# Optimization experiments

Hardware: AMD Instinct MI355X
Metric: run time of the kernel (lower is better)

Reference implementation:

```python
import jax, jax.numpy as jnp
import numpy as np

B, S, D = 2, 2048, 1024
H = 16
DH = D // H
DFF = 4096
EPS = 1e-5


def _layer_norm(x, gamma, beta):
    mu = jnp.mean(x, axis=-1, keepdims=True)
    var = jnp.mean(jnp.square(x - mu), axis=-1, keepdims=True)
    return (x - mu) * jax.lax.rsqrt(var + EPS) * gamma + beta


def setup_inputs() -> dict:
    key = jax.random.key(0)
    ks = jax.random.split(key, 8)
    sc_d = 1.0 / np.sqrt(D)
    sc_f = 1.0 / np.sqrt(DFF)
    x = jax.random.normal(ks[0], (B, S, D), dtype=jnp.float32)
    mask = jnp.ones((B, 1, 1, S), dtype=jnp.int32)
    # attention projections (stored as (in, out); y = x @ W + b)
    Wq = jax.random.normal(ks[1], (D, D), dtype=jnp.float32) * sc_d
    Wk = jax.random.normal(ks[2], (D, D), dtype=jnp.float32) * sc_d
    Wv = jax.random.normal(ks[3], (D, D), dtype=jnp.float32) * sc_d
    Wo = jax.random.normal(ks[4], (D, D), dtype=jnp.float32) * sc_d
    bq = jnp.zeros((D,), jnp.float32)
    bk = jnp.zeros((D,), jnp.float32)
    bv = jnp.zeros((D,), jnp.float32)
    bo = jnp.zeros((D,), jnp.float32)
    # feed-forward
    W0 = jax.random.normal(ks[5], (D, DFF), dtype=jnp.float32) * sc_d
    b0 = jnp.zeros((DFF,), jnp.float32)
    W1 = jax.random.normal(ks[6], (DFF, D), dtype=jnp.float32) * sc_f
    b1 = jnp.zeros((D,), jnp.float32)
    # layer norms
    g0 = jnp.ones((D,), jnp.float32)
    be0 = jnp.zeros((D,), jnp.float32)
    g1 = jnp.ones((D,), jnp.float32)
    be1 = jnp.zeros((D,), jnp.float32)
    return dict(x=x, mask=mask, Wq=Wq, bq=bq, Wk=Wk, bk=bk, Wv=Wv, bv=bv,
                Wo=Wo, bo=bo, W0=W0, b0=b0, W1=W1, b1=b1,
                g0=g0, be0=be0, g1=g1, be1=be1)


def reference(x, mask, Wq, bq, Wk, bk, Wv, bv, Wo, bo, W0, b0, W1, b1, g0, be0, g1, be1):
    b, s, d = x.shape
    # --- multi-head self-attention ---
    q = (x @ Wq + bq).reshape(b, s, H, DH).transpose(0, 2, 1, 3)  # (b,h,s,dh)
    k = (x @ Wk + bk).reshape(b, s, H, DH).transpose(0, 2, 1, 3)
    v = (x @ Wv + bv).reshape(b, s, H, DH).transpose(0, 2, 1, 3)
    scores = jnp.einsum('bhqd,bhkd->bhqk', q, k) / np.sqrt(DH)  # (b,h,s,s)
    scores = jnp.where(mask == 0, jnp.float32(-1e9), scores)
    probs = jax.nn.softmax(scores, axis=-1)
    ctx = jnp.einsum('bhqk,bhkd->bhqd', probs, v)
    ctx = ctx.transpose(0, 2, 1, 3).reshape(b, s, d)
    attn_out = ctx @ Wo + bo
    # dropout is identity in eval mode
    h0 = _layer_norm(x + attn_out, g0, be0)
    # --- feed-forward ---
    ff = jax.nn.relu(h0 @ W0 + b0) @ W1 + b1
    return _layer_norm(h0 + ff, g1, be1)
```

## Files before the change

kernel.cpp:

```cpp
#include <hip/hip_runtime.h>
#include <stdint.h>

#define B_ 2
#define S_ 2048
#define D_ 1024
#define H_ 16
#define DH_ 64
#define DFF_ 4096
#define NROW_ (B_*S_)
#define KVB_ 64

typedef __attribute__((ext_vector_type(8))) short bf16x8;
typedef __attribute__((ext_vector_type(4))) float f32x4;
typedef __attribute__((ext_vector_type(16))) float f32x16;
typedef __attribute__((ext_vector_type(4))) unsigned int u32x4;

__device__ __forceinline__ float bf2f(unsigned short u) {
  union { unsigned int i; float f; } v; v.i = ((unsigned int)u) << 16; return v.f;
}
__device__ __forceinline__ unsigned short f2bf(float f) {
  union { float f; unsigned int i; } v; v.f = f;
  unsigned int r = v.i + 0x7fffu + ((v.i >> 16) & 1u);
  return (unsigned short)(r >> 16);
}

__device__ __forceinline__ void gload16(const void* g, void* l) {
  __builtin_amdgcn_global_load_lds(
      (const __attribute__((address_space(1))) unsigned int*)(uintptr_t)g,
      (__attribute__((address_space(3))) unsigned int*)(unsigned int)(uintptr_t)l,
      16, 0, 0);
}

__device__ __forceinline__ void xcd_swz(int& bx, int& by) {
  const int gx = gridDim.x, nwg = gx * gridDim.y;
  const int flat = blockIdx.y * gx + blockIdx.x;
  const int chunk = nwg >> 3;
  const int nf = (flat & 7) * chunk + (flat >> 3);
  bx = nf % gx; by = nf / gx;
}

__global__ __launch_bounds__(256)
void k_cvt(const float* __restrict__ in, unsigned short* __restrict__ out, int n) {
  int i = (blockIdx.x * 256 + threadIdx.x) * 4;
  if (i < n) {
    float4 f = *(const float4*)(in + i);
    ushort4 o; o.x = f2bf(f.x); o.y = f2bf(f.y); o.z = f2bf(f.z); o.w = f2bf(f.w);
    *(ushort4*)(out + i) = o;
  }
}

__global__ __launch_bounds__(256)
void k_cat3(const float* __restrict__ a, const float* __restrict__ b,
            const float* __restrict__ c, float* __restrict__ o) {
  int i = blockIdx.x * 256 + threadIdx.x;
  if (i < 3 * D_)
    o[i] = i < D_ ? a[i] : (i < 2 * D_ ? b[i - D_] : c[i - 2 * D_]);
}

__global__ __launch_bounds__(256)
void k_cvt_t(const float* __restrict__ in, unsigned short* __restrict__ out,
             int K, int N) {
  __shared__ float tile[32][33];
  const int k0 = blockIdx.y * 32, n0 = blockIdx.x * 32;
  const int tx = threadIdx.x & 31, ty = threadIdx.x >> 5;
  #pragma unroll
  for (int i = 0; i < 32; i += 8)
    tile[ty + i][tx] = in[(size_t)(k0 + ty + i) * N + n0 + tx];
  __syncthreads();
  #pragma unroll
  for (int i = 0; i < 32; i += 8)
    out[(size_t)(n0 + ty + i) * K + k0 + tx] = f2bf(tile[tx][ty + i]);
}

__global__ __launch_bounds__(256)
void k_tr_v(const unsigned short* __restrict__ v, unsigned short* __restrict__ vt) {
  __shared__ unsigned short tile[32][33];
  const int b = blockIdx.z;
  const int s0 = blockIdx.y * 32, c0 = blockIdx.x * 32;
  const int tx = threadIdx.x & 31, ty = threadIdx.x >> 5;
  #pragma unroll
  for (int i = 0; i < 32; i += 8)
    tile[ty + i][tx] = v[((size_t)(b * S_ + s0 + ty + i)) * D_ + c0 + tx];
  __syncthreads();
  #pragma unroll
  for (int i = 0; i < 32; i += 8)
    vt[((size_t)(b * D_ + c0 + ty + i)) * S_ + s0 + tx] = tile[tx][ty + i];
}

template<int EPI>
__global__ __launch_bounds__(256, 2)
void k_gemm(const unsigned short* __restrict__ A,
            const unsigned short* __restrict__ Bt,
            const float* __restrict__ bias,
            void* __restrict__ out, int M, int N, int K) {
  __shared__ unsigned short Al[128 * 64];
  __shared__ unsigned short Bl[128 * 64];
  const int tid = threadIdx.x;
  const int wave = tid >> 6, l = tid & 63;
  int bx, by; xcd_swz(bx, by);
  const int m0 = by * 128, n0 = bx * 128;
  const int wm = (wave >> 1) * 64, wn = (wave & 1) * 64;
  const int g = l >> 4, c = l & 15;
  f32x4 acc[4][4] = {};
  const int srow = wave * 8 + (l >> 3);
  const int scol = (l & 7) * 8;

  for (int kt = 0; kt < K; kt += 64) {
    #pragma unroll
    for (int p = 0; p < 4; ++p) {
      const int r = p * 32 + srow;
      gload16(A + (size_t)(m0 + r) * K + kt + scol, Al + r * 64 + scol);
      gload16(Bt + (size_t)(n0 + r) * K + kt + scol, Bl + r * 64 + scol);
    }
    __syncthreads();
    #pragma unroll
    for (int ks = 0; ks < 2; ++ks) {
      bf16x8 af[4], bf[4];
      #pragma unroll
      for (int i = 0; i < 4; ++i) {
        af[i] = *(const bf16x8*)(Al + (wm + i * 16 + c) * 64 + ks * 32 + g * 8);
        bf[i] = *(const bf16x8*)(Bl + (wn + i * 16 + c) * 64 + ks * 32 + g * 8);
      }
      #pragma unroll
      for (int i = 0; i < 4; ++i)
        #pragma unroll
        for (int j = 0; j < 4; ++j)
          acc[i][j] = __builtin_amdgcn_mfma_f32_16x16x32_bf16(af[i], bf[j], acc[i][j], 0, 0, 0);
    }
    __syncthreads();
  }

  #pragma unroll
  for (int j = 0; j < 4; ++j) {
    const int col = n0 + wn + j * 16 + c;
    const float bv = bias[col];
    #pragma unroll
    for (int i = 0; i < 4; ++i) {
      #pragma unroll
      for (int r = 0; r < 4; ++r) {
        const int row = m0 + wm + i * 16 + g * 4 + r;
        float v = acc[i][j][r] + bv;
        if (EPI == 1) v = v > 0.f ? v : 0.f;
        if (EPI == 2) {
          ((float*)out)[(size_t)row * N + col] = v;
        } else if (EPI == 3) {
          ((unsigned short*)out)[(size_t)(col >> 10) * ((size_t)NROW_ * D_) +
                                 (size_t)row * D_ + (col & (D_ - 1))] = f2bf(v);
        } else {
          ((unsigned short*)out)[(size_t)row * N + col] = f2bf(v);
        }
      }
    }
  }
}

__global__ __launch_bounds__(256, 2)
void k_gemm_sk(const unsigned short* __restrict__ A,
               const unsigned short* __restrict__ Bt,
               const float* __restrict__ bias,
               unsigned short* __restrict__ out, int M, int N, int K, int KCH) {
  __shared__ unsigned short Al[128 * 64];
  __shared__ unsigned short Bl[128 * 64];
  const int tid = threadIdx.x;
  const int wave = tid >> 6, l = tid & 63;
  int bx, by; xcd_swz(bx, by);
  const int m0 = by * 128, n0 = bx * 128;
  const int kbeg = blockIdx.z * KCH;
  const int wm = (wave >> 1) * 64, wn = (wave & 1) * 64;
  const int g = l >> 4, c = l & 15;
  f32x4 acc[4][4] = {};
  const int srow = wave * 8 + (l >> 3);
  const int scol = (l & 7) * 8;

  for (int kt = kbeg; kt < kbeg + KCH; kt += 64) {
    #pragma unroll
    for (int p = 0; p < 4; ++p) {
      const int r = p * 32 + srow;
      gload16(A + (size_t)(m0 + r) * K + kt + scol, Al + r * 64 + scol);
      gload16(Bt + (size_t)(n0 + r) * K + kt + scol, Bl + r * 64 + scol);
    }
    __syncthreads();
    #pragma unroll
    for (int ks = 0; ks < 2; ++ks) {
      bf16x8 af[4], bf[4];
      #pragma unroll
      for (int i = 0; i < 4; ++i) {
        af[i] = *(const bf16x8*)(Al + (wm + i * 16 + c) * 64 + ks * 32 + g * 8);
        bf[i] = *(const bf16x8*)(Bl + (wn + i * 16 + c) * 64 + ks * 32 + g * 8);
      }
      #pragma unroll
      for (int i = 0; i < 4; ++i)
        #pragma unroll
        for (int j = 0; j < 4; ++j)
          acc[i][j] = __builtin_amdgcn_mfma_f32_16x16x32_bf16(af[i], bf[j], acc[i][j], 0, 0, 0);
    }
    __syncthreads();
  }

  unsigned short* op = out + (size_t)blockIdx.z * M * N;
  #pragma unroll
  for (int j = 0; j < 4; ++j) {
    const int col = n0 + wn + j * 16 + c;
    const float bv = (blockIdx.z == 0) ? bias[col] : 0.f;
    #pragma unroll
    for (int i = 0; i < 4; ++i) {
      #pragma unroll
      for (int r = 0; r < 4; ++r) {
        const int row = m0 + wm + i * 16 + g * 4 + r;
        op[(size_t)row * N + col] = f2bf(acc[i][j][r] + bv);
      }
    }
  }
}

__global__ __launch_bounds__(256, 2)
void k_attn(const unsigned short* __restrict__ q,
            const unsigned short* __restrict__ k,
            const unsigned short* __restrict__ vt,
            unsigned short* __restrict__ ctx) {
  __shared__ unsigned short Kl[2][64 * 64];
  __shared__ unsigned short Vl[2][64 * 64];
  const int tid = threadIdx.x, wave = tid >> 6, l = tid & 63;
  const int bh = blockIdx.y, b = bh >> 4, h = bh & 15;
  const int q0 = blockIdx.x * 128 + wave * 32;
  const int c32 = l & 31, hi = l >> 5;

  const unsigned short* qp = q + ((size_t)(b * S_ + q0 + c32)) * D_ + h * DH_ + hi * 8;
  bf16x8 qf[4];
  #pragma unroll
  for (int ks = 0; ks < 4; ++ks) qf[ks] = *(const bf16x8*)(qp + ks * 16);

  const unsigned short* kbase = k + ((size_t)(b * S_)) * D_ + h * DH_;
  const unsigned short* vbase = vt + ((size_t)bh) * DH_ * S_;
  const int o1 = tid * 16, o2 = tid * 16 + 4096;
  const int r1 = o1 >> 7, cb1 = (o1 & 127) ^ ((r1 & 7) << 4);
  const int r2 = o2 >> 7, cb2 = (o2 & 127) ^ ((r2 & 7) << 4);

  f32x16 acc0 = {}, acc1 = {};
  float l_r = 0.f;

  auto stage = [&](int bufi, int kv0) {
    unsigned short* Kb = &Kl[bufi][0];
    unsigned short* Vb = &Vl[bufi][0];
    gload16(kbase + (size_t)(kv0 + r1) * D_ + (cb1 >> 1), Kb + (o1 >> 1));
    gload16(kbase + (size_t)(kv0 + r2) * D_ + (cb2 >> 1), Kb + (o2 >> 1));
    gload16(vbase + (size_t)r1 * S_ + kv0 + (cb1 >> 1), Vb + (o1 >> 1));
    gload16(vbase + (size_t)r2 * S_ + kv0 + (cb2 >> 1), Vb + (o2 >> 1));
  };

  stage(0, 0);
  int cur = 0;
  for (int kv0 = 0; kv0 < S_; kv0 += KVB_) {
    __syncthreads();
    if (kv0 + KVB_ < S_) stage(cur ^ 1, kv0 + KVB_);
    const unsigned short* Kb = &Kl[cur][0];
    const unsigned short* Vb = &Vl[cur][0];

    f32x16 s0 = {}, s1 = {};
    __builtin_amdgcn_s_setprio(1);
    #pragma unroll
    for (int ks = 0; ks < 4; ++ks) {
      const int row0 = c32, row1 = 32 + c32;
      const int db = ks * 32 + hi * 16;
      bf16x8 kf0 = *(const bf16x8*)((const char*)Kb + row0 * 128 + (db ^ ((row0 & 7) << 4)));
      bf16x8 kf1 = *(const bf16x8*)((const char*)Kb + row1 * 128 + (db ^ ((row1 & 7) << 4)));
      s0 = __builtin_amdgcn_mfma_f32_32x32x16_bf16(kf0, qf[ks], s0, 0, 0, 0);
      s1 = __builtin_amdgcn_mfma_f32_32x32x16_bf16(kf1, qf[ks], s1, 0, 0, 0);
    }
    __builtin_amdgcn_s_setprio(0);

    #pragma unroll
    for (int r = 0; r < 16; ++r) {
      s0[r] = __expf(fminf(s0[r], 240.f) * 0.125f);
      s1[r] = __expf(fminf(s1[r], 240.f) * 0.125f);
    }
    float sm = 0.f;
    #pragma unroll
    for (int r = 0; r < 16; ++r) sm += s0[r] + s1[r];
    sm += __shfl_xor(sm, 32);
    l_r += sm;

    unsigned int W0[8], W1[8];
    #pragma unroll
    for (int i = 0; i < 8; ++i) {
      asm("v_cvt_pk_bf16_f32 %0, %1, %2" : "=v"(W0[i]) : "v"(s0[2 * i]), "v"(s0[2 * i + 1]));
      asm("v_cvt_pk_bf16_f32 %0, %1, %2" : "=v"(W1[i]) : "v"(s1[2 * i]), "v"(s1[2 * i + 1]));
    }
    #pragma unroll
    for (int kk = 0; kk < 2; ++kk) {
      asm volatile("v_permlane32_swap_b32 %0, %1" : "+v"(W0[4 * kk]), "+v"(W0[4 * kk + 2]));
      asm volatile("v_permlane32_swap_b32 %0, %1" : "+v"(W0[4 * kk + 1]), "+v"(W0[4 * kk + 3]));
      asm volatile("v_permlane32_swap_b32 %0, %1" : "+v"(W1[4 * kk]), "+v"(W1[4 * kk + 2]));
      asm volatile("v_permlane32_swap_b32 %0, %1" : "+v"(W1[4 * kk + 1]), "+v"(W1[4 * kk + 3]));
    }

    __builtin_amdgcn_s_setprio(1);
    #pragma unroll
    for (int ks = 0; ks < 4; ++ks) {
      union { unsigned int u[4]; bf16x8 v; } pk;
      const unsigned int* Wt = (ks < 2) ? W0 : W1;
      const int base = (ks & 1) * 4;
      pk.u[0] = Wt[base]; pk.u[1] = Wt[base + 1];
      pk.u[2] = Wt[base + 2]; pk.u[3] = Wt[base + 3];
      const int row0 = c32, row1 = 32 + c32;
      const int db = ks * 32 + hi * 16;
      bf16x8 vf0 = *(const bf16x8*)((const char*)Vb + row0 * 128 + (db ^ ((row0 & 7) << 4)));
      bf16x8 vf1 = *(const bf16x8*)((const char*)Vb + row1 * 128 + (db ^ ((row1 & 7) << 4)));
      acc0 = __builtin_amdgcn_mfma_f32_32x32x16_bf16(pk.v, vf0, acc0, 0, 0, 0);
      acc1 = __builtin_amdgcn_mfma_f32_32x32x16_bf16(pk.v, vf1, acc1, 0, 0, 0);
    }
    __builtin_amdgcn_s_setprio(0);
    cur ^= 1;
  }

  #pragma unroll
  for (int r = 0; r < 16; ++r) {
    const int qq = (r & 3) + 8 * (r >> 2) + 4 * hi;
    const float lv = __shfl(l_r, qq);
    const float inv = 1.0f / lv;
    const size_t rowb = ((size_t)(b * S_ + q0 + qq)) * D_ + h * DH_ + c32;
    ctx[rowb]      = f2bf(acc0[r] * inv);
    ctx[rowb + 32] = f2bf(acc1[r] * inv);
  }
}

template<int MODE>
__global__ __launch_bounds__(256)
void k_ln(const void* __restrict__ res, const unsigned short* __restrict__ y0,
          const unsigned short* __restrict__ y1,
          const float* __restrict__ gamma, const float* __restrict__ beta,
          void* __restrict__ out) {
  const int row = blockIdx.x, tid = threadIdx.x;
  const size_t base = (size_t)row * D_ + tid * 4;
  ushort4 ya = *(const ushort4*)(y0 + base);
  ushort4 yb = *(const ushort4*)(y1 + base);
  float h[4];
  if (MODE == 0) {
    float4 xv = *(const float4*)((const float*)res + base);
    h[0] = xv.x + bf2f(ya.x) + bf2f(yb.x); h[1] = xv.y + bf2f(ya.y) + bf2f(yb.y);
    h[2] = xv.z + bf2f(ya.z) + bf2f(yb.z); h[3] = xv.w + bf2f(ya.w) + bf2f(yb.w);
  } else {
    ushort4 xv = *(const ushort4*)((const unsigned short*)res + base);
    h[0] = bf2f(xv.x) + bf2f(ya.x) + bf2f(yb.x); h[1] = bf2f(xv.y) + bf2f(ya.y) + bf2f(yb.y);
    h[2] = bf2f(xv.z) + bf2f(ya.z) + bf2f(yb.z); h[3] = bf2f(xv.w) + bf2f(ya.w) + bf2f(yb.w);
  }
  float s = h[0] + h[1] + h[2] + h[3];
  float q = h[0]*h[0] + h[1]*h[1] + h[2]*h[2] + h[3]*h[3];
  #pragma unroll
  for (int m = 1; m < 64; m <<= 1) { s += __shfl_xor(s, m); q += __shfl_xor(q, m); }
  __shared__ float red[8];
  if ((tid & 63) == 0) { red[tid >> 6] = s; red[4 + (tid >> 6)] = q; }
  __syncthreads();
  s = red[0] + red[1] + red[2] + red[3];
  q = red[4] + red[5] + red[6] + red[7];
  const float mu = s * (1.0f / D_);
  const float rstd = rsqrtf(q * (1.0f / D_) - mu * mu + 1e-5f);
  const int c0 = tid * 4;
  float4 gv = *(const float4*)(gamma + c0);
  float4 bv = *(const float4*)(beta + c0);
  float o0 = (h[0] - mu) * rstd * gv.x + bv.x;
  float o1 = (h[1] - mu) * rstd * gv.y + bv.y;
  float o2 = (h[2] - mu) * rstd * gv.z + bv.z;
  float o3 = (h[3] - mu) * rstd * gv.w + bv.w;
  if (MODE == 0) {
    ushort4 ov; ov.x = f2bf(o0); ov.y = f2bf(o1); ov.z = f2bf(o2); ov.w = f2bf(o3);
    *(ushort4*)((unsigned short*)out + base) = ov;
  } else {
    float4 ov; ov.x = o0; ov.y = o1; ov.z = o2; ov.w = o3;
    *(float4*)((float*)out + base) = ov;
  }
}

extern "C" void kernel_launch(void* const* d_in, const int* in_sizes, int n_in,
                              void* d_out, int out_size, void* d_ws, size_t ws_size,
                              hipStream_t stream) {
  const float* x   = (const float*)d_in[0];
  const float* Wq  = (const float*)d_in[2];
  const float* bq  = (const float*)d_in[3];
  const float* Wk  = (const float*)d_in[4];
  const float* bk  = (const float*)d_in[5];
  const float* Wv  = (const float*)d_in[6];
  const float* bv  = (const float*)d_in[7];
  const float* Wo  = (const float*)d_in[8];
  const float* bo  = (const float*)d_in[9];
  const float* W0  = (const float*)d_in[10];
  const float* b0  = (const float*)d_in[11];
  const float* W1  = (const float*)d_in[12];
  const float* b1  = (const float*)d_in[13];
  const float* g0  = (const float*)d_in[14];
  const float* be0 = (const float*)d_in[15];
  const float* g1  = (const float*)d_in[16];
  const float* be1 = (const float*)d_in[17];

  char* ws = (char*)d_ws;
  const size_t MB = 1024 * 1024;
  unsigned short* xb   = (unsigned short*)(ws);
  unsigned short* vtb  = (unsigned short*)(ws);
  unsigned short* wqT  = (unsigned short*)(ws + 8 * MB);
  unsigned short* woT  = (unsigned short*)(ws + 14 * MB);
  unsigned short* w0T  = (unsigned short*)(ws + 16 * MB);
  unsigned short* w1T  = (unsigned short*)(ws + 24 * MB);
  unsigned short* qb   = (unsigned short*)(ws + 32 * MB);
  unsigned short* kb   = (unsigned short*)(ws + 40 * MB);
  unsigned short* vb   = (unsigned short*)(ws + 48 * MB);
  unsigned short* ctxb = (unsigned short*)(ws + 56 * MB);
  unsigned short* ap   = (unsigned short*)(ws + 32 * MB);
  unsigned short* h0b  = (unsigned short*)(ws + 48 * MB);
  unsigned short* ff1  = (unsigned short*)(ws + 56 * MB);
  unsigned short* fp   = (unsigned short*)(ws);
  float*          bcat = (float*)(ws + 64 * MB);

  k_cvt<<<4096, 256, 0, stream>>>(x, xb, NROW_ * D_);
  k_cat3<<<12, 256, 0, stream>>>(bq, bk, bv, bcat);
  k_cvt_t<<<dim3(32, 32), 256, 0, stream>>>(Wq, wqT, D_, D_);
  k_cvt_t<<<dim3(32, 32), 256, 0, stream>>>(Wk, wqT + (size_t)D_ * D_, D_, D_);
  k_cvt_t<<<dim3(32, 32), 256, 0, stream>>>(Wv, wqT + 2 * (size_t)D_ * D_, D_, D_);
  k_cvt_t<<<dim3(32, 32), 256, 0, stream>>>(Wo, woT, D_, D_);
  k_cvt_t<<<dim3(128, 32), 256, 0, stream>>>(W0, w0T, D_, DFF_);
  k_cvt_t<<<dim3(32, 128), 256, 0, stream>>>(W1, w1T, DFF_, D_);

  k_gemm<3><<<dim3(3 * D_ / 128, NROW_ / 128), 256, 0, stream>>>(
      xb, wqT, bcat, qb, NROW_, 3 * D_, D_);

  k_tr_v<<<dim3(D_ / 32, S_ / 32, B_), 256, 0, stream>>>(vb, vtb);

  k_attn<<<dim3(S_ / 128, B_ * H_), 256, 0, stream>>>(qb, kb, vtb, ctxb);

  k_gemm_sk<<<dim3(D_ / 128, NROW_ / 128, 2), 256, 0, stream>>>(
      ctxb, woT, bo, ap, NROW_, D_, D_, D_ / 2);
  k_ln<0><<<NROW_, 256, 0, stream>>>(x, ap, ap + (size_t)NROW_ * D_, g0, be0, h0b);

  k_gemm<1><<<dim3(DFF_ / 128, NROW_ / 128), 256, 0, stream>>>(
      h0b, w0T, b0, ff1, NROW_, DFF_, D_);
  k_gemm_sk<<<dim3(D_ / 128, NROW_ / 128, 2), 256, 0, stream>>>(
      ff1, w1T, b1, fp, NROW_, D_, DFF_, DFF_ / 2);
  k_ln<1><<<NROW_, 256, 0, stream>>>(h0b, fp, fp + (size_t)NROW_ * D_, g1, be1, (float*)d_out);

  (void)vtb; (void)ws_size; (void)n_in; (void)in_sizes; (void)out_size;
}
```

Measured before the change: 266.9 us.

## Widen attention KV tile to 128, fold softmax scale into Q projection

The attention kernel now stages 128 keys per iteration instead of 64. This halves the number of loop iterations and barriers, and each wave issues more MFMAs per synchronisation. The 1/sqrt(dh) scale moves into the QKV GEMM epilogue and the clamp before exp is dropped, which removes a multiply and a min per score element. Both GEMM kernels also raise their launch_bounds occupancy hint from 2 to 4, which may force register spilling. LDS use and register pressure in the attention kernel roughly double, and dropping the clamp relies on the scores staying small enough not to overflow exp.

```diff
diff --git a/kernel.cpp b/kernel.cpp
--- a/kernel.cpp
+++ b/kernel.cpp
@@ -8,7 +8,7 @@
 #define DH_ 64
 #define DFF_ 4096
 #define NROW_ (B_*S_)
-#define KVB_ 64
+#define KVB_ 128
 
 typedef __attribute__((ext_vector_type(8))) short bf16x8;
 typedef __attribute__((ext_vector_type(4))) float f32x4;
@@ -88,7 +88,7 @@
 }
 
 template<int EPI>
-__global__ __launch_bounds__(256, 2)
+__global__ __launch_bounds__(256, 4)
 void k_gemm(const unsigned short* __restrict__ A,
             const unsigned short* __restrict__ Bt,
             const float* __restrict__ bias,
@@ -144,6 +144,7 @@
         if (EPI == 2) {
           ((float*)out)[(size_t)row * N + col] = v;
         } else if (EPI == 3) {
+          if (col < D_) v *= 0.125f;
           ((unsigned short*)out)[(size_t)(col >> 10) * ((size_t)NROW_ * D_) +
                                  (size_t)row * D_ + (col & (D_ - 1))] = f2bf(v);
         } else {
@@ -154,7 +155,7 @@
   }
 }
 
-__global__ __launch_bounds__(256, 2)
+__global__ __launch_bounds__(256, 4)
 void k_gemm_sk(const unsigned short* __restrict__ A,
                const unsigned short* __restrict__ Bt,
                const float* __restrict__ bias,
@@ -218,8 +219,8 @@
             const unsigned short* __restrict__ k,
             const unsigned short* __restrict__ vt,
             unsigned short* __restrict__ ctx) {
-  __shared__ unsigned short Kl[2][64 * 64];
-  __shared__ unsigned short Vl[2][64 * 64];
+  __shared__ unsigned short Kl[2][128 * 64];
+  __shared__ unsigned short Vl[2][64 * 128];
   const int tid = threadIdx.x, wave = tid >> 6, l = tid & 63;
   const int bh = blockIdx.y, b = bh >> 4, h = bh & 15;
   const int q0 = blockIdx.x * 128 + wave * 32;
@@ -232,9 +233,6 @@
 
   const unsigned short* kbase = k + ((size_t)(b * S_)) * D_ + h * DH_;
   const unsigned short* vbase = vt + ((size_t)bh) * DH_ * S_;
-  const int o1 = tid * 16, o2 = tid * 16 + 4096;
-  const int r1 = o1 >> 7, cb1 = (o1 & 127) ^ ((r1 & 7) << 4);
-  const int r2 = o2 >> 7, cb2 = (o2 & 127) ^ ((r2 & 7) << 4);
 
   f32x16 acc0 = {}, acc1 = {};
   float l_r = 0.f;
@@ -242,10 +240,14 @@
   auto stage = [&](int bufi, int kv0) {
     unsigned short* Kb = &Kl[bufi][0];
     unsigned short* Vb = &Vl[bufi][0];
-    gload16(kbase + (size_t)(kv0 + r1) * D_ + (cb1 >> 1), Kb + (o1 >> 1));
-    gload16(kbase + (size_t)(kv0 + r2) * D_ + (cb2 >> 1), Kb + (o2 >> 1));
-    gload16(vbase + (size_t)r1 * S_ + kv0 + (cb1 >> 1), Vb + (o1 >> 1));
-    gload16(vbase + (size_t)r2 * S_ + kv0 + (cb2 >> 1), Vb + (o2 >> 1));
+    #pragma unroll
+    for (int p = 0; p < 4; ++p) {
+      const int o = tid * 16 + p * 4096;
+      const int kr = o >> 7, kc = (o & 127) ^ ((kr & 7) << 4);
+      gload16(kbase + (size_t)(kv0 + kr) * D_ + (kc >> 1), Kb + (o >> 1));
+      const int vr = o >> 8, vc = (o & 255) ^ ((vr & 7) << 4);
+      gload16(vbase + (size_t)vr * S_ + kv0 + (vc >> 1), Vb + (o >> 1));
+    }
   };
 
   stage(0, 0);
@@ -253,59 +255,60 @@
   for (int kv0 = 0; kv0 < S_; kv0 += KVB_) {
     __syncthreads();
     if (kv0 + KVB_ < S_) stage(cur ^ 1, kv0 + KVB_);
-    const unsigned short* Kb = &Kl[cur][0];
-    const unsigned short* Vb = &Vl[cur][0];
-
-    f32x16 s0 = {}, s1 = {};
+    const char* Kb = (const char*)&Kl[cur][0];
+    const char* Vb = (const char*)&Vl[cur][0];
+
+    f32x16 s[4] = {};
     __builtin_amdgcn_s_setprio(1);
     #pragma unroll
-    for (int ks = 0; ks < 4; ++ks) {
-      const int row0 = c32, row1 = 32 + c32;
-      const int db = ks * 32 + hi * 16;
-      bf16x8 kf0 = *(const bf16x8*)((const char*)Kb + row0 * 128 + (db ^ ((row0 & 7) << 4)));
-      bf16x8 kf1 = *(const bf16x8*)((const char*)Kb + row1 * 128 + (db ^ ((row1 & 7) << 4)));
-      s0 = __builtin_amdgcn_mfma_f32_32x32x16_bf16(kf0, qf[ks], s0, 0, 0, 0);
-      s1 = __builtin_amdgcn_mfma_f32_32x32x16_bf16(kf1, qf[ks], s1, 0, 0, 0);
+    for (int t = 0; t < 4; ++t) {
+      const int row = t * 32 + c32;
+      const int sw = (row & 7) << 4;
+      #pragma unroll
+      for (int ks = 0; ks < 4; ++ks) {
+        bf16x8 kf = *(const bf16x8*)(Kb + row * 128 + ((ks * 32 + hi * 16) ^ sw));
+        s[t] = __builtin_amdgcn_mfma_f32_32x32x16_bf16(kf, qf[ks], s[t], 0, 0, 0);
+      }
     }
     __builtin_amdgcn_s_setprio(0);
 
-    #pragma unroll
-    for (int r = 0; r < 16; ++r) {
-      s0[r] = __expf(fminf(s0[r], 240.f) * 0.125f);
-      s1[r] = __expf(fminf(s1[r], 240.f) * 0.125f);
-    }
-    float sm = 0.f;
-    #pragma unroll
-    for (int r = 0; r < 16; ++r) sm += s0[r] + s1[r];
+    float psum[4] = {0.f, 0.f, 0.f, 0.f};
+    #pragma unroll
+    for (int t = 0; t < 4; ++t)
+      #pragma unroll
+      for (int r = 0; r < 16; ++r) {
+        s[t][r] = __expf(s[t][r]);
+        psum[t] += s[t][r];
+      }
+    float sm = (psum[0] + psum[1]) + (psum[2] + psum[3]);
     sm += __shfl_xor(sm, 32);
     l_r += sm;
 
-    unsigned int W0[8], W1[8];
-    #pragma unroll
-    for (int i = 0; i < 8; ++i) {
-      asm("v_cvt_pk_bf16_f32 %0, %1, %2" : "=v"(W0[i]) : "v"(s0[2 * i]), "v"(s0[2 * i + 1]));
-      asm("v_cvt_pk_bf16_f32 %0, %1, %2" : "=v"(W1[i]) : "v"(s1[2 * i]), "v"(s1[2 * i + 1]));
-    }
-    #pragma unroll
-    for (int kk = 0; kk < 2; ++kk) {
-      asm volatile("v_permlane32_swap_b32 %0, %1" : "+v"(W0[4 * kk]), "+v"(W0[4 * kk + 2]));
-      asm volatile("v_permlane32_swap_b32 %0, %1" : "+v"(W0[4 * kk + 1]), "+v"(W0[4 * kk + 3]));
-      asm volatile("v_permlane32_swap_b32 %0, %1" : "+v"(W1[4 * kk]), "+v"(W1[4 * kk + 2]));
-      asm volatile("v_permlane32_swap_b32 %0, %1" : "+v"(W1[4 * kk + 1]), "+v"(W1[4 * kk + 3]));
+    unsigned int W[4][8];
+    #pragma unroll
+    for (int t = 0; t < 4; ++t) {
+      #pragma unroll
+      for (int i = 0; i < 8; ++i)
+        asm("v_cvt_pk_bf16_f32 %0, %1, %2"
+            : "=v"(W[t][i]) : "v"(s[t][2 * i]), "v"(s[t][2 * i + 1]));
+      #pragma unroll
+      for (int kk = 0; kk < 2; ++kk) {
+        asm volatile("v_permlane32_swap_b32 %0, %1" : "+v"(W[t][4*kk]),   "+v"(W[t][4*kk+2]));
+        asm volatile("v_permlane32_swap_b32 %0, %1" : "+v"(W[t][4*kk+1]), "+v"(W[t][4*kk+3]));
+      }
     }
 
     __builtin_amdgcn_s_setprio(1);
     #pragma unroll
-    for (int ks = 0; ks < 4; ++ks) {
+    for (int m = 0; m < 8; ++m) {
+      const int t = m >> 1, kk = m & 1;
       union { unsigned int u[4]; bf16x8 v; } pk;
-      const unsigned int* Wt = (ks < 2) ? W0 : W1;
-      const int base = (ks & 1) * 4;
-      pk.u[0] = Wt[base]; pk.u[1] = Wt[base + 1];
-      pk.u[2] = Wt[base + 2]; pk.u[3] = Wt[base + 3];
+      pk.u[0] = W[t][4*kk]; pk.u[1] = W[t][4*kk+1];
+      pk.u[2] = W[t][4*kk+2]; pk.u[3] = W[t][4*kk+3];
       const int row0 = c32, row1 = 32 + c32;
-      const int db = ks * 32 + hi * 16;
-      bf16x8 vf0 = *(const bf16x8*)((const char*)Vb + row0 * 128 + (db ^ ((row0 & 7) << 4)));
-      bf16x8 vf1 = *(const bf16x8*)((const char*)Vb + row1 * 128 + (db ^ ((row1 & 7) << 4)));
+      const int db = m * 32 + hi * 16;
+      bf16x8 vf0 = *(const bf16x8*)(Vb + row0 * 256 + (db ^ ((row0 & 7) << 4)));
+      bf16x8 vf1 = *(const bf16x8*)(Vb + row1 * 256 + (db ^ ((row1 & 7) << 4)));
       acc0 = __builtin_amdgcn_mfma_f32_32x32x16_bf16(pk.v, vf0, acc0, 0, 0, 0);
       acc1 = __builtin_amdgcn_mfma_f32_32x32x16_bf16(pk.v, vf1, acc1, 0, 0, 0);
     }
```

New measurement: 245.4 us. -8.1%, faster.
